# Kernel tuning notes

Measured on AMD Instinct MI355X. Metric: run time of the kernel, lower is better.

Reference implementation:

```python
import jax, jax.numpy as jnp
import numpy as np

N = 8192      # nb_nodes
HID = 128     # hid_dim
OUT = 64      # out_dim
E = 262144    # num edges (avg degree 32)
BN_EPS = 1e-5


def setup_inputs() -> dict:
    key = jax.random.key(0)
    ks = jax.random.split(key, 10)
    x = jax.random.normal(ks[0], (N, HID), dtype=jnp.float32)
    adj = jnp.zeros((N, N), dtype=jnp.float32)  # unused by the module's forward
    src = jax.random.randint(ks[1], (E,), 0, N)
    dst = jax.random.randint(ks[2], (E,), 0, N)
    s = 0.05
    fc_w = jax.random.normal(ks[3], (HID, OUT), dtype=jnp.float32) * s
    fc_b = jnp.zeros((OUT,), dtype=jnp.float32)
    w1 = jax.random.normal(ks[4], (HID, HID), dtype=jnp.float32) * s
    w1_b = jnp.zeros((HID,), dtype=jnp.float32)
    w2 = jax.random.normal(ks[5], (HID, OUT), dtype=jnp.float32) * s
    w2_b = jnp.zeros((OUT,), dtype=jnp.float32)
    epsilon = jnp.full((N,), 0.5, dtype=jnp.float32)  # init.constant_(0.5)
    gamma = jnp.ones((OUT,), dtype=jnp.float32)
    beta = jnp.zeros((OUT,), dtype=jnp.float32)
    return {"x": x, "adj": adj, "src": src, "dst": dst,
            "fc_w": fc_w, "fc_b": fc_b, "w1": w1, "w1_b": w1_b,
            "w2": w2, "w2_b": w2_b, "epsilon": epsilon,
            "gamma": gamma, "beta": beta}


def _neighbor_sum(feat, src, dst):
    # DGL copy_src + sum: each dst node sums features of its src neighbors.
    return jax.ops.segment_sum(feat[src], dst, num_segments=N)


def reference(x, adj, src, dst, fc_w, fc_b, w1, w1_b, w2, w2_b, epsilon, gamma, beta):
    # h1 = fc(x)
    h1 = x @ fc_w + fc_b                                  # [N, OUT]
    # layer1: neighbor-sum then linear, ReLU
    h2 = jax.nn.relu(_neighbor_sum(x, src, dst) @ w1 + w1_b)   # [N, HID]
    # layer2: neighbor-sum then linear
    h2 = _neighbor_sum(h2, src, dst) @ w2 + w2_b          # [N, OUT]
    eps = epsilon[:, None]
    h = (1.0 - eps) * h1 + eps * h2                       # [N, OUT]
    ret = (h @ h.T + x @ x.T) * 0.5                       # [N, N]
    # BatchNorm1d (training mode: batch stats, biased variance)
    mean = jnp.mean(h, axis=0)
    var = jnp.var(h, axis=0)
    h_bn = (h - mean) * jax.lax.rsqrt(var + BN_EPS) * gamma + beta
    return ret, h_bn
```

## Files before the change

### kernel.cpp

```cpp
#include <hip/hip_runtime.h>
#include <hip/hip_bf16.h>

#define N_NODES 8192
#define HID 128
#define OUT_F 64
#define E_EDGES 262144
#define KTOT 192
#define LDK 104

typedef __bf16 bf16x8 __attribute__((ext_vector_type(8)));
typedef float  f32x4  __attribute__((ext_vector_type(4)));

__device__ __forceinline__ unsigned short f2bf(float f) {
    unsigned int u = __float_as_uint(f);
    u += 0x7fffu + ((u >> 16) & 1u);
    return (unsigned short)(u >> 16);
}

__global__ void count_k(const int* __restrict__ dst, int* __restrict__ cnt) {
    int e = blockIdx.x * 256 + threadIdx.x;
    if (e < E_EDGES) atomicAdd(&cnt[dst[e]], 1);
}

__global__ void scan_k(const int* __restrict__ cnt, int* __restrict__ off,
                       int* __restrict__ cursor, float* __restrict__ stats) {
    __shared__ int part[256];
    int tid = threadIdx.x;
    if (tid < 128) stats[tid] = 0.0f;
    int base = tid * 32;
    int local[32];
    int s = 0;
    #pragma unroll
    for (int j = 0; j < 32; ++j) { local[j] = s; s += cnt[base + j]; }
    part[tid] = s;
    __syncthreads();
    if (tid == 0) {
        int acc = 0;
        for (int i = 0; i < 256; ++i) { int t = part[i]; part[i] = acc; acc += t; }
    }
    __syncthreads();
    int p = part[tid];
    #pragma unroll
    for (int j = 0; j < 32; ++j) {
        int v = p + local[j];
        off[base + j] = v;
        cursor[base + j] = v;
    }
    if (tid == 255) off[N_NODES] = p + s;
}

__global__ void fill_k(const int* __restrict__ src, const int* __restrict__ dst,
                       int* __restrict__ cursor, int* __restrict__ eidx) {
    int e = blockIdx.x * 256 + threadIdx.x;
    if (e >= E_EDGES) return;
    int pos = atomicAdd(&cursor[dst[e]], 1);
    eidx[pos] = src[e];
}

__global__ __launch_bounds__(256)
void pre_k(const float* __restrict__ x,
           const float* __restrict__ fcw, const float* __restrict__ fcb,
           const float* __restrict__ w1,
           float* __restrict__ h1, float* __restrict__ y,
           unsigned short* __restrict__ G) {
    __shared__ float wS[64 * 192];
    __shared__ float xs[16 * HID];
    int tid = threadIdx.x;
    int rowbase = blockIdx.x * 16;

    for (int i = tid; i < 512; i += 256)
        *(float4*)&xs[i * 4] = *(const float4*)&x[(size_t)rowbase * HID + i * 4];

    int c = tid & 63, r0 = tid >> 6;
    float acc[3][4] = {};

    for (int kh = 0; kh < 2; ++kh) {
        __syncthreads();
        for (int i = tid; i < 1024; i += 256) {
            int k = i >> 4, qd = i & 15;
            *(float4*)&wS[k * 192 + qd * 4] =
                *(const float4*)&fcw[(size_t)(kh * 64 + k) * 64 + qd * 4];
        }
        for (int i = tid; i < 2048; i += 256) {
            int k = i >> 5, qd = i & 31;
            *(float4*)&wS[k * 192 + 64 + qd * 4] =
                *(const float4*)&w1[(size_t)(kh * 64 + k) * 128 + qd * 4];
        }
        __syncthreads();
        #pragma unroll 4
        for (int k = 0; k < 64; ++k) {
            float wa = wS[k * 192 + c];
            float wb = wS[k * 192 + 64 + c];
            float wc = wS[k * 192 + 128 + c];
            #pragma unroll
            for (int g = 0; g < 4; ++g) {
                float xv = xs[(r0 + 4 * g) * HID + kh * 64 + k];
                acc[0][g] += xv * wa;
                acc[1][g] += xv * wb;
                acc[2][g] += xv * wc;
            }
        }
    }
    float b = fcb[c];
    #pragma unroll
    for (int g = 0; g < 4; ++g) {
        int r = rowbase + r0 + 4 * g;
        h1[(size_t)r * OUT_F + c]    = acc[0][g] + b;
        y[(size_t)r * HID + c]       = acc[1][g];
        y[(size_t)r * HID + 64 + c]  = acc[2][g];
    }
    const float SC = 0.70710678f;
    for (int i = tid; i < 2048; i += 256) {
        int r = i >> 7, cc = i & 127;
        G[(size_t)(rowbase + r) * KTOT + OUT_F + cc] = f2bf(xs[r * HID + cc] * SC);
    }
}

__global__ void gather_relu_k(const float* __restrict__ feat,
                              const int* __restrict__ eidx,
                              const int* __restrict__ off,
                              const float* __restrict__ bias,
                              float* __restrict__ out) {
    int node = blockIdx.x * 4 + (threadIdx.x >> 6);
    int lane = threadIdx.x & 63;
    int beg = off[node], end = off[node + 1];
    float2 a0{0,0}, a1{0,0}, a2{0,0}, a3{0,0}, a4{0,0}, a5{0,0}, a6{0,0}, a7{0,0};
    int j = beg;
    for (; j + 8 <= end; j += 8) {
        int s0 = eidx[j],     s1 = eidx[j + 1], s2 = eidx[j + 2], s3 = eidx[j + 3];
        int s4 = eidx[j + 4], s5 = eidx[j + 5], s6 = eidx[j + 6], s7 = eidx[j + 7];
        float2 v0 = *((const float2*)(feat + (size_t)s0 * HID) + lane);
        float2 v1 = *((const float2*)(feat + (size_t)s1 * HID) + lane);
        float2 v2 = *((const float2*)(feat + (size_t)s2 * HID) + lane);
        float2 v3 = *((const float2*)(feat + (size_t)s3 * HID) + lane);
        float2 v4 = *((const float2*)(feat + (size_t)s4 * HID) + lane);
        float2 v5 = *((const float2*)(feat + (size_t)s5 * HID) + lane);
        float2 v6 = *((const float2*)(feat + (size_t)s6 * HID) + lane);
        float2 v7 = *((const float2*)(feat + (size_t)s7 * HID) + lane);
        a0.x += v0.x; a0.y += v0.y;  a1.x += v1.x; a1.y += v1.y;
        a2.x += v2.x; a2.y += v2.y;  a3.x += v3.x; a3.y += v3.y;
        a4.x += v4.x; a4.y += v4.y;  a5.x += v5.x; a5.y += v5.y;
        a6.x += v6.x; a6.y += v6.y;  a7.x += v7.x; a7.y += v7.y;
    }
    for (; j < end; ++j) {
        int s0 = eidx[j];
        float2 v0 = *((const float2*)(feat + (size_t)s0 * HID) + lane);
        a0.x += v0.x; a0.y += v0.y;
    }
    float2 r;
    r.x = ((a0.x + a1.x) + (a2.x + a3.x)) + ((a4.x + a5.x) + (a6.x + a7.x));
    r.y = ((a0.y + a1.y) + (a2.y + a3.y)) + ((a4.y + a5.y) + (a6.y + a7.y));
    float2 bb = *((const float2*)bias + lane);
    r.x = fmaxf(r.x + bb.x, 0.0f);
    r.y = fmaxf(r.y + bb.y, 0.0f);
    *((float2*)(out + (size_t)node * HID) + lane) = r;
}

__global__ __launch_bounds__(256)
void mlp2_k(const float* __restrict__ h2, const float* __restrict__ w2,
            float* __restrict__ z) {
    __shared__ float wS[HID * 64];
    __shared__ float xs[16 * HID];
    int tid = threadIdx.x;
    int rowbase = blockIdx.x * 16;
    for (int i = tid; i < 512; i += 256)
        *(float4*)&xs[i * 4] = *(const float4*)&h2[(size_t)rowbase * HID + i * 4];
    for (int i = tid; i < 2048; i += 256)
        *(float4*)&wS[i * 4] = *(const float4*)&w2[i * 4];
    __syncthreads();
    int c = tid & 63, r0 = tid >> 6;
    float acc[4] = {};
    #pragma unroll 4
    for (int k = 0; k < HID; ++k) {
        float wv = wS[k * 64 + c];
        #pragma unroll
        for (int g = 0; g < 4; ++g)
            acc[g] += xs[(r0 + 4 * g) * HID + k] * wv;
    }
    #pragma unroll
    for (int g = 0; g < 4; ++g)
        z[(size_t)(rowbase + r0 + 4 * g) * OUT_F + c] = acc[g];
}

__global__ void gather_fuse_k(const float* __restrict__ z,
                              const int* __restrict__ eidx,
                              const int* __restrict__ off,
                              const float* __restrict__ h1,
                              const float* __restrict__ w2b,
                              const float* __restrict__ eps,
                              float* __restrict__ h,
                              unsigned short* __restrict__ G,
                              float* __restrict__ stats) {
    __shared__ float red[8][64];
    int tid = threadIdx.x;
    int wid = tid >> 6, lane = tid & 63;
    float s = 0.0f, q = 0.0f;
    float b = w2b[lane];
    const float SC = 0.70710678f;
    for (int t = 0; t < 4; ++t) {
        int node = blockIdx.x * 16 + wid * 4 + t;
        int beg = off[node], end = off[node + 1];
        float a0 = 0, a1 = 0, a2 = 0, a3 = 0, a4 = 0, a5 = 0, a6 = 0, a7 = 0;
        int j = beg;
        for (; j + 8 <= end; j += 8) {
            int s0 = eidx[j],     s1 = eidx[j + 1], s2 = eidx[j + 2], s3 = eidx[j + 3];
            int s4 = eidx[j + 4], s5 = eidx[j + 5], s6 = eidx[j + 6], s7 = eidx[j + 7];
            a0 += z[(size_t)s0 * OUT_F + lane];
            a1 += z[(size_t)s1 * OUT_F + lane];
            a2 += z[(size_t)s2 * OUT_F + lane];
            a3 += z[(size_t)s3 * OUT_F + lane];
            a4 += z[(size_t)s4 * OUT_F + lane];
            a5 += z[(size_t)s5 * OUT_F + lane];
            a6 += z[(size_t)s6 * OUT_F + lane];
            a7 += z[(size_t)s7 * OUT_F + lane];
        }
        for (; j < end; ++j)
            a0 += z[(size_t)eidx[j] * OUT_F + lane];
        float gs = ((a0 + a1) + (a2 + a3)) + ((a4 + a5) + (a6 + a7));
        float e = eps[node];
        float hv = (1.0f - e) * h1[(size_t)node * OUT_F + lane] + e * (gs + b);
        h[(size_t)node * OUT_F + lane] = hv;
        G[(size_t)node * KTOT + lane] = f2bf(hv * SC);
        s += hv;
        q += hv * hv;
    }
    red[wid][lane] = s;
    red[4 + wid][lane] = q;
    __syncthreads();
    if (tid < 64) {
        atomicAdd(&stats[tid],
                  (red[0][tid] + red[1][tid]) + (red[2][tid] + red[3][tid]));
    } else if (tid < 128) {
        int l = tid - 64;
        atomicAdd(&stats[64 + l],
                  (red[4][l] + red[5][l]) + (red[6][l] + red[7][l]));
    }
}

__global__ void bn_apply_k(const float* __restrict__ h,
                           const float* __restrict__ stats,
                           const float* __restrict__ gamma,
                           const float* __restrict__ beta,
                           float* __restrict__ outBN) {
    int idx = blockIdx.x * 256 + threadIdx.x;
    if (idx >= N_NODES * OUT_F) return;
    int c = idx & 63;
    const float inv_n = 1.0f / 8192.0f;
    float m = stats[c] * inv_n;
    float v = stats[64 + c] * inv_n - m * m;
    outBN[idx] = (h[idx] - m) * rsqrtf(v + 1e-5f) * gamma[c] + beta[c];
}

__global__ __launch_bounds__(256, 2)
void big_gemm_k(const unsigned short* __restrict__ G, float* __restrict__ C) {
    int bx = blockIdx.x, by = blockIdx.y;
    if (bx > by) return;
    __shared__ unsigned short Ap[128 * LDK];
    __shared__ unsigned short Bp[128 * LDK];
    int tid = threadIdx.x;
    int lane = tid & 63, wid = tid >> 6;
    int wm = wid >> 1, wn = wid & 1;
    int row0 = by * 128, col0 = bx * 128;

    f32x4 acc[4][4] = {};

    #pragma unroll
    for (int kh = 0; kh < 2; ++kh) {
        for (int i = tid; i < 128 * 12; i += 256) {
            int r = i / 12, cc = i % 12;
            *(uint4*)(&Ap[r * LDK + cc * 8]) =
                *(const uint4*)(G + (size_t)(row0 + r) * KTOT + kh * 96 + cc * 8);
            *(uint4*)(&Bp[r * LDK + cc * 8]) =
                *(const uint4*)(G + (size_t)(col0 + r) * KTOT + kh * 96 + cc * 8);
        }
        __syncthreads();
        int rA = wm * 64 + (lane & 15);
        int rB = wn * 64 + (lane & 15);
        int klane = (lane >> 4) * 8;
        #pragma unroll
        for (int ks = 0; ks < 3; ++ks) {
            bf16x8 af[4], bfr[4];
            #pragma unroll
            for (int t = 0; t < 4; ++t) {
                af[t]  = *(const bf16x8*)(&Ap[(rA + t * 16) * LDK + ks * 32 + klane]);
                bfr[t] = *(const bf16x8*)(&Bp[(rB + t * 16) * LDK + ks * 32 + klane]);
            }
            #pragma unroll
            for (int tm = 0; tm < 4; ++tm)
                #pragma unroll
                for (int tn = 0; tn < 4; ++tn)
                    acc[tm][tn] = __builtin_amdgcn_mfma_f32_16x16x32_bf16(
                        af[tm], bfr[tn], acc[tm][tn], 0, 0, 0);
        }
        __syncthreads();
    }

    int crow = row0 + wm * 64 + (lane >> 4) * 4;
    int ccol = col0 + wn * 64 + (lane & 15);
    #pragma unroll
    for (int tm = 0; tm < 4; ++tm)
        #pragma unroll
        for (int tn = 0; tn < 4; ++tn)
            #pragma unroll
            for (int r = 0; r < 4; ++r)
                C[(size_t)(crow + tm * 16 + r) * N_NODES + (ccol + tn * 16)] =
                    acc[tm][tn][r];

    if (bx != by) {
        int trow = col0 + wn * 64 + (lane & 15);
        int tcol = row0 + wm * 64 + (lane >> 4) * 4;
        #pragma unroll
        for (int tm = 0; tm < 4; ++tm)
            #pragma unroll
            for (int tn = 0; tn < 4; ++tn)
                *(float4*)&C[(size_t)(trow + tn * 16) * N_NODES + tcol + tm * 16] =
                    *(const float4*)&acc[tm][tn];
    }
}

extern "C" void kernel_launch(void* const* d_in, const int* in_sizes, int n_in,
                              void* d_out, int out_size, void* d_ws, size_t ws_size,
                              hipStream_t stream) {
    const float* x    = (const float*)d_in[0];
    const int*   src  = (const int*)d_in[2];
    const int*   dst  = (const int*)d_in[3];
    const float* fcw  = (const float*)d_in[4];
    const float* fcb  = (const float*)d_in[5];
    const float* w1   = (const float*)d_in[6];
    const float* w1b  = (const float*)d_in[7];
    const float* w2   = (const float*)d_in[8];
    const float* w2b  = (const float*)d_in[9];
    const float* eps  = (const float*)d_in[10];
    const float* gamma= (const float*)d_in[11];
    const float* beta = (const float*)d_in[12];

    float* ws = (float*)d_ws;
    float* y     = ws;
    float* h2    = ws + 1048576;
    float* h1    = ws + 2097152;
    float* z     = ws + 2621440;
    float* h     = ws + 3145728;
    unsigned short* G = (unsigned short*)(ws + 3670016);
    float* stats = ws + 3670016 + 786432;
    int*   cnt    = (int*)(ws + 3670016 + 786432 + 128);
    int*   off    = cnt + N_NODES;
    int*   cursor = off + N_NODES + 1;
    int*   eidx   = cursor + N_NODES;

    float* ret   = (float*)d_out;
    float* outBN = (float*)d_out + (size_t)N_NODES * N_NODES;

    hipMemsetAsync(cnt, 0, N_NODES * sizeof(int), stream);

    dim3 blk(256);

    count_k<<<E_EDGES / 256, blk, 0, stream>>>(dst, cnt);
    scan_k<<<1, blk, 0, stream>>>(cnt, off, cursor, stats);
    fill_k<<<E_EDGES / 256, blk, 0, stream>>>(src, dst, cursor, eidx);

    pre_k<<<N_NODES / 16, blk, 0, stream>>>(x, fcw, fcb, w1, h1, y, G);
    gather_relu_k<<<N_NODES / 4, blk, 0, stream>>>(y, eidx, off, w1b, h2);
    mlp2_k<<<N_NODES / 16, blk, 0, stream>>>(h2, w2, z);
    gather_fuse_k<<<N_NODES / 16, blk, 0, stream>>>(z, eidx, off, h1, w2b, eps,
                                                    h, G, stats);
    bn_apply_k<<<(N_NODES * OUT_F) / 256, blk, 0, stream>>>(h, stats, gamma, beta, outBN);
    dim3 grid(64, 64);
    big_gemm_k<<<grid, blk, 0, stream>>>(G, ret);
}
```

Before: 529.2 us.

## Fuse gather-ReLU with second MLP and restructure symmetric GEMM launch and stores

```diff
diff --git a/kernel.cpp b/kernel.cpp
--- a/kernel.cpp
+++ b/kernel.cpp
@@ -6,7 +6,6 @@
 #define OUT_F 64
 #define E_EDGES 262144
 #define KTOT 192
-#define LDK 104
 
 typedef __bf16 bf16x8 __attribute__((ext_vector_type(8)));
 typedef float  f32x4  __attribute__((ext_vector_type(4)));
@@ -116,13 +115,22 @@
     }
 }
 
-__global__ void gather_relu_k(const float* __restrict__ feat,
-                              const int* __restrict__ eidx,
-                              const int* __restrict__ off,
-                              const float* __restrict__ bias,
-                              float* __restrict__ out) {
-    int node = blockIdx.x * 4 + (threadIdx.x >> 6);
-    int lane = threadIdx.x & 63;
+__global__ __launch_bounds__(256)
+void gather_mlp_k(const float* __restrict__ feat,
+                  const int* __restrict__ eidx,
+                  const int* __restrict__ off,
+                  const float* __restrict__ bias,
+                  const float* __restrict__ w2,
+                  float* __restrict__ z) {
+    __shared__ float wS[HID * 64];
+    __shared__ float rowS[4][HID];
+    int tid = threadIdx.x;
+    int wid = tid >> 6, lane = tid & 63;
+
+    for (int i = tid; i < 2048; i += 256)
+        *(float4*)&wS[i * 4] = *(const float4*)&w2[i * 4];
+
+    int node = blockIdx.x * 4 + wid;
     int beg = off[node], end = off[node + 1];
     float2 a0{0,0}, a1{0,0}, a2{0,0}, a3{0,0}, a4{0,0}, a5{0,0}, a6{0,0}, a7{0,0};
     int j = beg;
@@ -151,35 +159,15 @@
     r.x = ((a0.x + a1.x) + (a2.x + a3.x)) + ((a4.x + a5.x) + (a6.x + a7.x));
     r.y = ((a0.y + a1.y) + (a2.y + a3.y)) + ((a4.y + a5.y) + (a6.y + a7.y));
     float2 bb = *((const float2*)bias + lane);
-    r.x = fmaxf(r.x + bb.x, 0.0f);
-    r.y = fmaxf(r.y + bb.y, 0.0f);
-    *((float2*)(out + (size_t)node * HID) + lane) = r;
-}
-
-__global__ __launch_bounds__(256)
-void mlp2_k(const float* __restrict__ h2, const float* __restrict__ w2,
-            float* __restrict__ z) {
-    __shared__ float wS[HID * 64];
-    __shared__ float xs[16 * HID];
-    int tid = threadIdx.x;
-    int rowbase = blockIdx.x * 16;
-    for (int i = tid; i < 512; i += 256)
-        *(float4*)&xs[i * 4] = *(const float4*)&h2[(size_t)rowbase * HID + i * 4];
-    for (int i = tid; i < 2048; i += 256)
-        *(float4*)&wS[i * 4] = *(const float4*)&w2[i * 4];
+    rowS[wid][lane * 2]     = fmaxf(r.x + bb.x, 0.0f);
+    rowS[wid][lane * 2 + 1] = fmaxf(r.y + bb.y, 0.0f);
     __syncthreads();
-    int c = tid & 63, r0 = tid >> 6;
-    float acc[4] = {};
-    #pragma unroll 4
-    for (int k = 0; k < HID; ++k) {
-        float wv = wS[k * 64 + c];
-        #pragma unroll
-        for (int g = 0; g < 4; ++g)
-            acc[g] += xs[(r0 + 4 * g) * HID + k] * wv;
-    }
-    #pragma unroll
-    for (int g = 0; g < 4; ++g)
-        z[(size_t)(rowbase + r0 + 4 * g) * OUT_F + c] = acc[g];
+
+    float acc = 0.0f;
+    #pragma unroll 8
+    for (int k = 0; k < HID; ++k)
+        acc += rowS[wid][k] * wS[k * 64 + lane];
+    z[(size_t)node * OUT_F + lane] = acc;
 }
 
 __global__ void gather_fuse_k(const float* __restrict__ z,
@@ -251,48 +239,40 @@
     outBN[idx] = (h[idx] - m) * rsqrtf(v + 1e-5f) * gamma[c] + beta[c];
 }
 
-__global__ __launch_bounds__(256, 2)
+__global__ __launch_bounds__(256, 4)
 void big_gemm_k(const unsigned short* __restrict__ G, float* __restrict__ C) {
-    int bx = blockIdx.x, by = blockIdx.y;
-    if (bx > by) return;
-    __shared__ unsigned short Ap[128 * LDK];
-    __shared__ unsigned short Bp[128 * LDK];
+    int bid = blockIdx.x;
+    int by = (int)((sqrtf(8.0f * bid + 1.0f) - 1.0f) * 0.5f);
+    while ((by + 1) * (by + 2) / 2 <= bid) ++by;
+    while (by * (by + 1) / 2 > bid) --by;
+    int bx = bid - by * (by + 1) / 2;
+
     int tid = threadIdx.x;
     int lane = tid & 63, wid = tid >> 6;
     int wm = wid >> 1, wn = wid & 1;
     int row0 = by * 128, col0 = bx * 128;
 
+    const unsigned short* Abase =
+        G + (size_t)(row0 + wm * 64 + (lane & 15)) * KTOT + (lane >> 4) * 8;
+    const unsigned short* Bbase =
+        G + (size_t)(col0 + wn * 64 + (lane & 15)) * KTOT + (lane >> 4) * 8;
+
     f32x4 acc[4][4] = {};
 
     #pragma unroll
-    for (int kh = 0; kh < 2; ++kh) {
-        for (int i = tid; i < 128 * 12; i += 256) {
-            int r = i / 12, cc = i % 12;
-            *(uint4*)(&Ap[r * LDK + cc * 8]) =
-                *(const uint4*)(G + (size_t)(row0 + r) * KTOT + kh * 96 + cc * 8);
-            *(uint4*)(&Bp[r * LDK + cc * 8]) =
-                *(const uint4*)(G + (size_t)(col0 + r) * KTOT + kh * 96 + cc * 8);
-        }
-        __syncthreads();
-        int rA = wm * 64 + (lane & 15);
-        int rB = wn * 64 + (lane & 15);
-        int klane = (lane >> 4) * 8;
+    for (int kk = 0; kk < 6; ++kk) {
+        bf16x8 af[4], bfr[4];
         #pragma unroll
-        for (int ks = 0; ks < 3; ++ks) {
-            bf16x8 af[4], bfr[4];
+        for (int t = 0; t < 4; ++t) {
+            af[t]  = *(const bf16x8*)(Abase + (size_t)t * 16 * KTOT + kk * 32);
+            bfr[t] = *(const bf16x8*)(Bbase + (size_t)t * 16 * KTOT + kk * 32);
+        }
+        #pragma unroll
+        for (int tm = 0; tm < 4; ++tm)
             #pragma unroll
-            for (int t = 0; t < 4; ++t) {
-                af[t]  = *(const bf16x8*)(&Ap[(rA + t * 16) * LDK + ks * 32 + klane]);
-                bfr[t] = *(const bf16x8*)(&Bp[(rB + t * 16) * LDK + ks * 32 + klane]);
-            }
-            #pragma unroll
-            for (int tm = 0; tm < 4; ++tm)
-                #pragma unroll
-                for (int tn = 0; tn < 4; ++tn)
-                    acc[tm][tn] = __builtin_amdgcn_mfma_f32_16x16x32_bf16(
-                        af[tm], bfr[tn], acc[tm][tn], 0, 0, 0);
-        }
-        __syncthreads();
+            for (int tn = 0; tn < 4; ++tn)
+                acc[tm][tn] = __builtin_amdgcn_mfma_f32_16x16x32_bf16(
+                    af[tm], bfr[tn], acc[tm][tn], 0, 0, 0);
     }
 
     int crow = row0 + wm * 64 + (lane >> 4) * 4;
@@ -303,8 +283,8 @@
         for (int tn = 0; tn < 4; ++tn)
             #pragma unroll
             for (int r = 0; r < 4; ++r)
-                C[(size_t)(crow + tm * 16 + r) * N_NODES + (ccol + tn * 16)] =
-                    acc[tm][tn][r];
+                __builtin_nontemporal_store(acc[tm][tn][r],
+                    &C[(size_t)(crow + tm * 16 + r) * N_NODES + (ccol + tn * 16)]);
 
     if (bx != by) {
         int trow = col0 + wn * 64 + (lane & 15);
@@ -312,9 +292,11 @@
         #pragma unroll
         for (int tm = 0; tm < 4; ++tm)
             #pragma unroll
-            for (int tn = 0; tn < 4; ++tn)
-                *(float4*)&C[(size_t)(trow + tn * 16) * N_NODES + tcol + tm * 16] =
-                    *(const float4*)&acc[tm][tn];
+            for (int tn = 0; tn < 4; ++tn) {
+                f32x4 v = acc[tm][tn];
+                __builtin_nontemporal_store(v,
+                    (f32x4*)&C[(size_t)(trow + tn * 16) * N_NODES + tcol + tm * 16]);
+            }
     }
 }
 
@@ -336,13 +318,12 @@
 
     float* ws = (float*)d_ws;
     float* y     = ws;
-    float* h2    = ws + 1048576;
-    float* h1    = ws + 2097152;
-    float* z     = ws + 2621440;
-    float* h     = ws + 3145728;
-    unsigned short* G = (unsigned short*)(ws + 3670016);
-    float* stats = ws + 3670016 + 786432;
-    int*   cnt    = (int*)(ws + 3670016 + 786432 + 128);
+    float* h1    = ws + 1048576;
+    float* z     = ws + 1572864;
+    float* h     = ws + 2097152;
+    unsigned short* G = (unsigned short*)(ws + 2621440);
+    float* stats = ws + 2621440 + 786432;
+    int*   cnt    = (int*)(ws + 3408000);
     int*   off    = cnt + N_NODES;
     int*   cursor = off + N_NODES + 1;
     int*   eidx   = cursor + N_NODES;
@@ -359,11 +340,9 @@
     fill_k<<<E_EDGES / 256, blk, 0, stream>>>(src, dst, cursor, eidx);
 
     pre_k<<<N_NODES / 16, blk, 0, stream>>>(x, fcw, fcb, w1, h1, y, G);
-    gather_relu_k<<<N_NODES / 4, blk, 0, stream>>>(y, eidx, off, w1b, h2);
-    mlp2_k<<<N_NODES / 16, blk, 0, stream>>>(h2, w2, z);
+    gather_mlp_k<<<N_NODES / 4, blk, 0, stream>>>(y, eidx, off, w1b, w2, z);
     gather_fuse_k<<<N_NODES / 16, blk, 0, stream>>>(z, eidx, off, h1, w2b, eps,
                                                     h, G, stats);
     bn_apply_k<<<(N_NODES * OUT_F) / 256, blk, 0, stream>>>(h, stats, gamma, beta, outBN);
-    dim3 grid(64, 64);
-    big_gemm_k<<<grid, blk, 0, stream>>>(G, ret);
-}
+    big_gemm_k<<<2080, blk, 0, stream>>>(G, ret);
+}
```

Result: slower. 569.9 us (+7.7%).
